# Performance work log

Hardware: AMD Instinct MI355X
Metric: run time of the kernel (lower is better)

Reference implementation:

```python
import jax, jax.numpy as jnp
import numpy as np

B, S, H = 2, 1024, 2048
NH, NKV, HD = 32, 8, 64
EPS = 1e-6
ROPE_BASE = 10000.0


def rms_norm(x, w, eps=EPS):
    xf = x.astype(jnp.float32)
    var = jnp.mean(xf * xf, axis=-1, keepdims=True)
    return (w * (xf * jax.lax.rsqrt(var + eps))).astype(x.dtype)


def rotate_half(x):
    x1, x2 = jnp.split(x, 2, axis=-1)
    return jnp.concatenate((-x2, x1), axis=-1)


def setup_inputs() -> dict:
    key = jax.random.key(0)
    ks = jax.random.split(key, 8)
    hidden_states = jax.random.normal(ks[0], (B, S, H), dtype=jnp.float32) * 0.02
    # real rotary embeddings for positions 0..S-1
    inv_freq = 1.0 / (ROPE_BASE ** (jnp.arange(0, HD, 2, dtype=jnp.float32) / HD))
    freqs = jnp.arange(S, dtype=jnp.float32)[:, None] * inv_freq[None, :]  # [S, HD/2]
    emb = jnp.concatenate((freqs, freqs), axis=-1)  # [S, HD]
    cos = jnp.broadcast_to(jnp.cos(emb)[None], (B, S, HD)).astype(jnp.float32)
    sin = jnp.broadcast_to(jnp.sin(emb)[None], (B, S, HD)).astype(jnp.float32)
    # additive causal mask [B, 1, S, S]
    causal = jnp.tril(jnp.ones((S, S), dtype=bool))
    attention_mask = jnp.broadcast_to(
        jnp.where(causal, 0.0, -1e9).astype(jnp.float32)[None, None], (B, 1, S, S))
    scale_in = 1.0 / np.sqrt(H)
    wq = jax.random.normal(ks[1], (H, NH * HD), dtype=jnp.float32) * scale_in
    wk = jax.random.normal(ks[2], (H, NKV * HD), dtype=jnp.float32) * scale_in
    wv = jax.random.normal(ks[3], (H, NKV * HD), dtype=jnp.float32) * scale_in
    wo = jax.random.normal(ks[4], (NH * HD, H), dtype=jnp.float32) * scale_in
    q_norm_w = jnp.ones((NH * HD,), dtype=jnp.float32)
    k_norm_w = jnp.ones((NKV * HD,), dtype=jnp.float32)
    return {"hidden_states": hidden_states, "cos": cos, "sin": sin,
            "attention_mask": attention_mask, "wq": wq, "wk": wk, "wv": wv,
            "wo": wo, "q_norm_w": q_norm_w, "k_norm_w": k_norm_w}


def reference(hidden_states, cos, sin, attention_mask, wq, wk, wv, wo, q_norm_w, k_norm_w):
    b, s, _ = hidden_states.shape
    scaling = HD ** -0.5
    groups = NH // NKV
    # projections + QK-norm (RMSNorm over full projected dim, before head split)
    q = rms_norm(hidden_states @ wq, q_norm_w)
    k = rms_norm(hidden_states @ wk, k_norm_w)
    v = hidden_states @ wv
    q = q.reshape(b, s, NH, HD).transpose(0, 2, 1, 3)   # [b, nh, s, hd]
    k = k.reshape(b, s, NKV, HD).transpose(0, 2, 1, 3)  # [b, nkv, s, hd]
    v = v.reshape(b, s, NKV, HD).transpose(0, 2, 1, 3)
    # RoPE (cos/sin broadcast over head dim)
    c = cos[:, None]  # [b, 1, s, hd]
    sn = sin[:, None]
    q = q * c + rotate_half(q) * sn
    k = k * c + rotate_half(k) * sn
    # GQA: repeat KV heads
    k = jnp.repeat(k, groups, axis=1)  # [b, nh, s, hd]
    v = jnp.repeat(v, groups, axis=1)
    scores = jnp.einsum('bhqd,bhkd->bhqk', q, k) * scaling + attention_mask
    attn = jax.nn.softmax(scores.astype(jnp.float32), axis=-1).astype(q.dtype)
    out = jnp.einsum('bhqk,bhkd->bhqd', attn, v)
    out = out.transpose(0, 2, 1, 3).reshape(b, s, NH * HD)
    return out @ wo
```

## Files before the change

kernel.cpp:

```cpp
#include <hip/hip_runtime.h>

#define B_    2
#define S_    1024
#define NH_   32
#define NKV_  8
#define T_    (B_*S_)

typedef unsigned short u16;
typedef unsigned int u32;
typedef __attribute__((ext_vector_type(8))) short bf16x8;
typedef __attribute__((ext_vector_type(4))) float f32x4;

__device__ __forceinline__ float bf2f(u16 u) {
    union { float f; unsigned int i; } c; c.i = ((unsigned int)u) << 16; return c.f;
}
__device__ __forceinline__ u16 f2bf(float f) {
    union { float f; unsigned int u; } c; c.f = f;
    return (u16)((c.u + 0x7FFFu + ((c.u >> 16) & 1u)) >> 16);
}

__device__ __forceinline__ void gld_lds16(const void* g, void* s) {
    __builtin_amdgcn_global_load_lds(
        (const __attribute__((address_space(1))) void*)g,
        (__attribute__((address_space(3))) void*)s,
        16, 0, 0);
}

__global__ __launch_bounds__(256) void preproc1(
    const float* __restrict__ hidden, const float* __restrict__ wq,
    const float* __restrict__ wk, const float* __restrict__ wv,
    const float* __restrict__ wo,
    u16* __restrict__ hidden_bf, u16* __restrict__ wqkvT, u16* __restrict__ woT)
{
    __shared__ float t[64][65];
    const int bid = blockIdx.x, tid = threadIdx.x;
    if (bid < 2048) {
        int i = (bid * 256 + tid) * 8;
        float4 v0 = *reinterpret_cast<const float4*>(&hidden[i]);
        float4 v1 = *reinterpret_cast<const float4*>(&hidden[i + 4]);
        u16 o[8] = { f2bf(v0.x), f2bf(v0.y), f2bf(v0.z), f2bf(v0.w),
                     f2bf(v1.x), f2bf(v1.y), f2bf(v1.z), f2bf(v1.w) };
        *reinterpret_cast<uint4*>(&hidden_bf[i]) = *reinterpret_cast<uint4*>(o);
        return;
    }
    const float* src; int scol, sN, n0, k0;
    u16* dst; int dK;
    if (bid < 3584) {
        const int tt = bid - 2048;
        n0 = (tt % 48) * 64; k0 = (tt / 48) * 64;
        if (n0 < 2048)      { src = wq; scol = n0;        sN = 2048; }
        else if (n0 < 2560) { src = wk; scol = n0 - 2048; sN = 512;  }
        else                { src = wv; scol = n0 - 2560; sN = 512;  }
        dst = wqkvT; dK = 2048;
    } else {
        const int tt = bid - 3584;
        n0 = (tt % 32) * 64; k0 = (tt / 32) * 64;
        src = wo; scol = n0; sN = 2048;
        dst = woT; dK = 2048;
    }
    #pragma unroll
    for (int i = 0; i < 16; ++i) {
        int e = i * 256 + tid, r = e >> 6, c = e & 63;
        t[r][c] = src[(size_t)(k0 + r) * sN + scol + c];
    }
    __syncthreads();
    #pragma unroll
    for (int i = 0; i < 16; ++i) {
        int e = i * 256 + tid, rr = e >> 6, cc = e & 63;
        dst[(size_t)(n0 + rr) * dK + k0 + cc] = f2bf(t[cc][rr]);
    }
}

template<bool OUT_BF16>
__global__ __launch_bounds__(256) void gemm_bt(
    const u16* __restrict__ A, const u16* __restrict__ Bt,
    void* __restrict__ Cv, int M, int N, int K)
{
    __shared__ u16 As[2][128 * 64];
    __shared__ u16 Bs[2][64 * 64];
    const int MB = M >> 7;
    const int cpx = gridDim.x >> 3;
    const int L = (blockIdx.x & 7) * cpx + (blockIdx.x >> 3);
    const int bm = (L % MB) * 128, bn = (L / MB) * 64;
    const int tid = threadIdx.x;
    const int w = tid >> 6, lane = tid & 63;
    const int wr = w >> 1, wc = w & 1;
    const int l15 = lane & 15, lg = lane >> 4;
    const int srow = lane >> 3;
    const int scolsw = (lane & 7) ^ srow;

    f32x4 acc[4][2] = {};
    const int nk = K >> 6;

#define GSTAGE(ks, bb) do {                                                    \
    const int kofs = (ks) * 64;                                                \
    _Pragma("unroll")                                                          \
    for (int i_ = 0; i_ < 4; ++i_) {                                           \
        int chunk_ = w * 4 + i_;                                               \
        int row_ = chunk_ * 8 + srow;                                          \
        gld_lds16(&A[(size_t)(bm + row_) * K + kofs + scolsw * 8],             \
                  &As[bb][chunk_ * 512]);                                      \
    }                                                                          \
    _Pragma("unroll")                                                          \
    for (int j_ = 0; j_ < 2; ++j_) {                                           \
        int chunk_ = w * 2 + j_;                                               \
        int row_ = chunk_ * 8 + srow;                                          \
        gld_lds16(&Bt[(size_t)(bn + row_) * K + kofs + scolsw * 8],            \
                  &Bs[bb][chunk_ * 512]);                                      \
    } } while (0)

    GSTAGE(0, 0);
    for (int ks = 0; ks < nk; ++ks) {
        const int cur = ks & 1;
        if (ks + 1 < nk) {
            GSTAGE(ks + 1, cur ^ 1);
            asm volatile("s_waitcnt vmcnt(6)" ::: "memory");
        } else {
            asm volatile("s_waitcnt vmcnt(0)" ::: "memory");
        }
        __builtin_amdgcn_sched_barrier(0);
        __builtin_amdgcn_s_barrier();
        __builtin_amdgcn_sched_barrier(0);

        #pragma unroll
        for (int kk = 0; kk < 2; ++kk) {
            const int phys = ((kk * 4 + lg) ^ (l15 & 7)) * 8;
            bf16x8 a[4], b[2];
            #pragma unroll
            for (int m = 0; m < 4; ++m)
                a[m] = *reinterpret_cast<const bf16x8*>(
                    &As[cur][(wr * 64 + m * 16 + l15) * 64 + phys]);
            #pragma unroll
            for (int n = 0; n < 2; ++n)
                b[n] = *reinterpret_cast<const bf16x8*>(
                    &Bs[cur][(wc * 32 + n * 16 + l15) * 64 + phys]);
            #pragma unroll
            for (int m = 0; m < 4; ++m)
                #pragma unroll
                for (int n = 0; n < 2; ++n)
                    acc[m][n] = __builtin_amdgcn_mfma_f32_16x16x32_bf16(
                        a[m], b[n], acc[m][n], 0, 0, 0);
        }
        __builtin_amdgcn_sched_barrier(0);
        __builtin_amdgcn_s_barrier();
    }
#undef GSTAGE

    const int orow0 = bm + wr * 64, ocol0 = bn + wc * 32;
    #pragma unroll
    for (int m = 0; m < 4; ++m)
        #pragma unroll
        for (int n = 0; n < 2; ++n)
            #pragma unroll
            for (int r = 0; r < 4; ++r) {
                int row = orow0 + m * 16 + lg * 4 + r;
                int col = ocol0 + n * 16 + l15;
                float v = acc[m][n][r];
                if (OUT_BF16)
                    ((u16*)Cv)[(size_t)row * N + col] = f2bf(v);
                else
                    ((float*)Cv)[(size_t)row * N + col] = v;
            }
}

template<int DIM>
__device__ __forceinline__ void rms_rope_row(
    u16* base, const float* __restrict__ w,
    const float* __restrict__ cs, const float* __restrict__ sn,
    float* row, float* red, int tid, float osc)
{
    float ss = 0.f;
    for (int i0 = tid * 8; i0 < DIM; i0 += 2048) {
        uint4 u = *reinterpret_cast<const uint4*>(&base[i0]);
        const u16* us = reinterpret_cast<const u16*>(&u);
        #pragma unroll
        for (int j = 0; j < 8; ++j) { float f = bf2f(us[j]); row[i0 + j] = f; ss += f * f; }
    }
    #pragma unroll
    for (int off = 1; off < 64; off <<= 1) ss += __shfl_xor(ss, off);
    if ((tid & 63) == 0) red[tid >> 6] = ss;
    __syncthreads();
    const float rstd = rsqrtf((red[0] + red[1] + red[2] + red[3]) * (1.0f / DIM) + 1e-6f);

    for (int i0 = tid * 8; i0 < DIM; i0 += 2048) {
        u16 o[8];
        #pragma unroll
        for (int j = 0; j < 8; ++j) {
            int i = i0 + j, dh = i & 63, bb = i & ~63;
            int oi = (dh < 32) ? bb + dh + 32 : bb + dh - 32;
            float y     = row[i]  * rstd * w[i];
            float other = row[oi] * rstd * w[oi];
            if (dh < 32) other = -other;
            o[j] = f2bf((y * cs[dh] + other * sn[dh]) * osc);
        }
        *reinterpret_cast<uint4*>(&base[i0]) = *reinterpret_cast<uint4*>(o);
    }
}

__global__ __launch_bounds__(256) void rmsnorm_rope_vt(
    u16* __restrict__ x, const float* __restrict__ qnw, const float* __restrict__ knw,
    const float* __restrict__ cosb, const float* __restrict__ sinb,
    u16* __restrict__ vT)
{
    __shared__ float smem[2304];
    const int bid = blockIdx.x, tid = threadIdx.x;
    if (bid < 2048) {
        const int t = bid;
        float* row = smem;
        float* red = smem + 2048;
        const float* cs = cosb + (size_t)t * 64;
        const float* sn = sinb + (size_t)t * 64;
        rms_rope_row<2048>(x + (size_t)t * 3072,        qnw, cs, sn, row, red, tid,
                           0.18033688f);
        __syncthreads();
        rms_rope_row<512 >(x + (size_t)t * 3072 + 2048, knw, cs, sn, row, red, tid,
                           1.0f);
        return;
    }
    u16 (*tu)[72] = reinterpret_cast<u16(*)[72]>(smem);
    const int bid2 = bid - 2048;
    const int hd = bid2 % 16;
    const int s0 = (bid2 / 16) * 64;
    const int b = hd >> 3, kvh = hd & 7;
    #pragma unroll
    for (int i = 0; i < 2; ++i) {
        int chunk = i * 256 + tid;
        int r = chunk >> 3, c8 = (chunk & 7) * 8;
        uint4 u = *reinterpret_cast<const uint4*>(
            &x[(size_t)(b * 1024 + s0 + r) * 3072 + 2560 + kvh * 64 + c8]);
        *reinterpret_cast<uint4*>(&tu[r][c8]) = u;
    }
    __syncthreads();
    #pragma unroll
    for (int i = 0; i < 2; ++i) {
        int chunk = i * 256 + tid;
        int d = chunk >> 3, c8 = (chunk & 7) * 8;
        u16 o[8];
        #pragma unroll
        for (int j = 0; j < 8; ++j) o[j] = tu[c8 + j][d];
        *reinterpret_cast<uint4*>(&vT[((size_t)(hd * 64 + d)) * 1024 + s0 + c8])
            = *reinterpret_cast<uint4*>(o);
    }
}

__global__ __launch_bounds__(256) void attn_tb(
    const u16* __restrict__ qkv,
    const u16* __restrict__ vT,
    u16* __restrict__ ob)
{
    __shared__ u16 Ks[3][64 * 64];
    __shared__ u16 Vs[3][64 * 64];
    __shared__ u16 Ps[4][16 * 64];

    const int bid = blockIdx.x;
    const int L   = (bid & 7) * 64 + (bid >> 3);
    const int g5  = L >> 5;
    const int rem = L & 31;
    const int ha  = rem & 3;
    const int p   = rem >> 2;
    const int b = g5 >> 3, kvh = g5 & 7;
    const int h = kvh * 4 + ha;
    const int qtA = p, qtB = 15 - p;

    const int tid = threadIdx.x, w = tid >> 6, lane = tid & 63;
    const int l15 = lane & 15, lg = lane >> 4;
    const int srow = lane >> 3;
    const int scolsw = (lane & 7) ^ srow;

    bf16x8 qfA[2], qfB[2];
    {
        const size_t rA = (size_t)(b * 1024 + qtA * 64 + w * 16 + l15);
        const size_t rB = (size_t)(b * 1024 + qtB * 64 + w * 16 + l15);
        #pragma unroll
        for (int kk = 0; kk < 2; ++kk) {
            qfA[kk] = *reinterpret_cast<const bf16x8*>(
                &qkv[rA * 3072 + h * 64 + kk * 32 + lg * 8]);
            qfB[kk] = *reinterpret_cast<const bf16x8*>(
                &qkv[rB * 3072 + h * 64 + kk * 32 + lg * 8]);
        }
    }
    asm volatile("s_waitcnt vmcnt(0)" ::: "memory");

    float lrA = 0.f, lrB = 0.f;
    f32x4 oaccA[4] = {}, oaccB[4] = {};

    const u16* kbase = qkv + 2048 + kvh * 64;
    const u16* vbase = vT + (size_t)(g5 * 64) * 1024;
    const int qgA = qtA * 64 + w * 16 + l15;
    const int qgB = qtB * 64 + w * 16 + l15;

#define ASTAGE(kt, bb) do {                                                    \
    _Pragma("unroll")                                                          \
    for (int i_ = 0; i_ < 2; ++i_) {                                           \
        int chunk_ = w * 2 + i_;                                               \
        int row_ = chunk_ * 8 + srow;                                          \
        gld_lds16(&kbase[(size_t)(b * 1024 + (kt) * 64 + row_) * 3072          \
                         + scolsw * 8], &Ks[bb][chunk_ * 512]);                \
        gld_lds16(&vbase[(size_t)row_ * 1024 + (kt) * 64 + scolsw * 8],        \
                  &Vs[bb][chunk_ * 512]);                                      \
    } } while (0)

    auto step = [&](int kt, int cur, const bf16x8 (&qf)[2],
                    float& lr, f32x4 (&oacc)[4], int qg, bool dz) {
        f32x4 sacc[4] = {};
        __builtin_amdgcn_s_setprio(1);
        #pragma unroll
        for (int kk = 0; kk < 2; ++kk) {
            const int phys = ((kk * 4 + lg) ^ (l15 & 7)) * 8;
            #pragma unroll
            for (int m = 0; m < 4; ++m) {
                bf16x8 kf = *reinterpret_cast<const bf16x8*>(
                    &Ks[cur][(m * 16 + l15) * 64 + phys]);
                sacc[m] = __builtin_amdgcn_mfma_f32_16x16x32_bf16(
                    kf, qf[kk], sacc[m], 0, 0, 0);
            }
        }
        __builtin_amdgcn_s_setprio(0);

        float ls = 0.f;
        #pragma unroll
        for (int m = 0; m < 4; ++m) {
            u16 pk[4];
            #pragma unroll
            for (int r = 0; r < 4; ++r) {
                float v = sacc[m][r];
                if (dz && (kt * 64 + m * 16 + lg * 4 + r > qg)) v = -1e30f;
                float e = exp2f(v);
                ls += e;
                pk[r] = f2bf(e);
            }
            const int keyc = m * 16 + lg * 4;
            const int phys = (keyc >> 3) ^ (l15 & 7);
            *reinterpret_cast<uint2*>(&Ps[w][l15 * 64 + phys * 8 + (keyc & 7)])
                = *reinterpret_cast<const uint2*>(pk);
        }
        lr += ls;

        __builtin_amdgcn_s_setprio(1);
        #pragma unroll
        for (int kk = 0; kk < 2; ++kk) {
            const int phys = ((kk * 4 + lg) ^ (l15 & 7)) * 8;
            bf16x8 pf = *reinterpret_cast<const bf16x8*>(
                &Ps[w][l15 * 64 + phys]);
            #pragma unroll
            for (int d = 0; d < 4; ++d) {
                bf16x8 vf = *reinterpret_cast<const bf16x8*>(
                    &Vs[cur][(d * 16 + l15) * 64 + phys]);
                oacc[d] = __builtin_amdgcn_mfma_f32_16x16x32_bf16(
                    pf, vf, oacc[d], 0, 0, 0);
            }
        }
        __builtin_amdgcn_s_setprio(0);
    };

    ASTAGE(0, 0);
    for (int s = 0; s <= 16; ++s) {
        const int cur = s % 3;
        if (s < 16) {
            const int ktn = (s + 1 <= p) ? (s + 1) : (s - p);
            ASTAGE(ktn, (s + 1) % 3);
            asm volatile("s_waitcnt vmcnt(4)" ::: "memory");
        } else {
            asm volatile("s_waitcnt vmcnt(0)" ::: "memory");
        }
        __builtin_amdgcn_sched_barrier(0);
        __builtin_amdgcn_s_barrier();
        __builtin_amdgcn_sched_barrier(0);

        if (s <= p) step(s,         cur, qfA, lrA, oaccA, qgA, s == p);
        else        step(s - p - 1, cur, qfB, lrB, oaccB, qgB, s == 16);
    }
#undef ASTAGE

    #pragma unroll
    for (int tt = 0; tt < 2; ++tt) {
        const int qt = tt ? qtB : qtA;
        float lsum = tt ? lrB : lrA;
        lsum += __shfl_xor(lsum, 16);
        lsum += __shfl_xor(lsum, 32);
        f32x4* oacc = tt ? oaccB : oaccA;
        float linv[4];
        #pragma unroll
        for (int r = 0; r < 4; ++r) {
            float lv = __shfl(lsum, (lane & 48) + ((lane >> 4) & 3) * 4 + r);
            linv[r] = 1.f / lv;
        }
        #pragma unroll
        for (int d = 0; d < 4; ++d)
            #pragma unroll
            for (int r = 0; r < 4; ++r)
                ob[(size_t)(b * 1024 + qt * 64 + w * 16 + lg * 4 + r) * 2048
                   + h * 64 + d * 16 + l15] = f2bf(oacc[d][r] * linv[r]);
    }
}

extern "C" void kernel_launch(void* const* d_in, const int* in_sizes, int n_in,
                              void* d_out, int out_size, void* d_ws, size_t ws_size,
                              hipStream_t stream)
{
    const float* hidden = (const float*)d_in[0];
    const float* cosb   = (const float*)d_in[1];
    const float* sinb   = (const float*)d_in[2];
    const float* wq     = (const float*)d_in[4];
    const float* wk     = (const float*)d_in[5];
    const float* wv     = (const float*)d_in[6];
    const float* wo     = (const float*)d_in[7];
    const float* qnw    = (const float*)d_in[8];
    const float* knw    = (const float*)d_in[9];
    float* out = (float*)d_out;

    char* ws = (char*)d_ws;
    u16* hidden_bf = (u16*)ws;
    u16* wqkvT     = (u16*)(ws + ((size_t)8  << 20));
    u16* attn_bf   = (u16*)(ws + ((size_t)8  << 20));
    u16* qkv_bf    = (u16*)(ws + ((size_t)20 << 20));
    u16* v_bfT     = (u16*)(ws + ((size_t)32 << 20));
    u16* woT       = (u16*)(ws + ((size_t)34 << 20));

    preproc1<<<4608, 256, 0, stream>>>(hidden, wq, wk, wv, wo,
                                       hidden_bf, wqkvT, woT);

    gemm_bt<true><<<768, 256, 0, stream>>>(hidden_bf, wqkvT, qkv_bf,
                                           2048, 3072, 2048);

    rmsnorm_rope_vt<<<2304, 256, 0, stream>>>(qkv_bf, qnw, knw, cosb, sinb, v_bfT);

    attn_tb<<<512, 256, 0, stream>>>(qkv_bf, v_bfT, attn_bf);

    gemm_bt<false><<<512, 256, 0, stream>>>(attn_bf, woT, out,
                                            2048, 2048, 2048);
}
```

Measured before the change: 125.2 us.

## Split attention KV loop into two halves with a separate merge kernel

The attention kernel's 17-step KV loop per block is split into two halves (steps 0-8 and 9-16), doubling the grid to 1024 blocks. Each half writes unnormalized fp32 partial outputs and row sums to workspace, and a new merge kernel adds them, normalizes, and converts to bf16. The K/V LDS ring shrinks from triple to double buffering, with an extra barrier per step. The aim is more parallelism and occupancy, at the cost of a large fp32 round trip through global memory and one more kernel launch.

```diff
diff --git a/kernel.cpp b/kernel.cpp
--- a/kernel.cpp
+++ b/kernel.cpp
@@ -243,24 +243,28 @@
     }
 }
 
-__global__ __launch_bounds__(256) void attn_tb(
+__global__ __launch_bounds__(256) void attn_split(
     const u16* __restrict__ qkv,
     const u16* __restrict__ vT,
-    u16* __restrict__ ob)
-{
-    __shared__ u16 Ks[3][64 * 64];
-    __shared__ u16 Vs[3][64 * 64];
+    float* __restrict__ opart,
+    float* __restrict__ lpart)
+{
+    __shared__ u16 Ks[2][64 * 64];
+    __shared__ u16 Vs[2][64 * 64];
     __shared__ u16 Ps[4][16 * 64];
 
     const int bid = blockIdx.x;
-    const int L   = (bid & 7) * 64 + (bid >> 3);
-    const int g5  = L >> 5;
-    const int rem = L & 31;
-    const int ha  = rem & 3;
-    const int p   = rem >> 2;
+    const int L    = (bid & 7) * 128 + (bid >> 3);
+    const int g5   = L >> 6;
+    const int rem  = L & 63;
+    const int ha   = rem & 3;
+    const int p    = (rem >> 2) & 7;
+    const int half = rem >> 5;
     const int b = g5 >> 3, kvh = g5 & 7;
     const int h = kvh * 4 + ha;
     const int qtA = p, qtB = 15 - p;
+    const int s0 = half ? 9 : 0;
+    const int s1 = half ? 17 : 9;
 
     const int tid = threadIdx.x, w = tid >> 6, lane = tid & 63;
     const int l15 = lane & 15, lg = lane >> 4;
@@ -353,12 +357,12 @@
         __builtin_amdgcn_s_setprio(0);
     };
 
-    ASTAGE(0, 0);
-    for (int s = 0; s <= 16; ++s) {
-        const int cur = s % 3;
-        if (s < 16) {
-            const int ktn = (s + 1 <= p) ? (s + 1) : (s - p);
-            ASTAGE(ktn, (s + 1) % 3);
+#define TILEOF(s) (((s) <= p) ? (s) : ((s) - p - 1))
+    ASTAGE(TILEOF(s0), s0 & 1);
+    for (int s = s0; s < s1; ++s) {
+        const int cur = s & 1;
+        if (s + 1 < s1) {
+            ASTAGE(TILEOF(s + 1), cur ^ 1);
             asm volatile("s_waitcnt vmcnt(4)" ::: "memory");
         } else {
             asm volatile("s_waitcnt vmcnt(0)" ::: "memory");
@@ -369,9 +373,15 @@
 
         if (s <= p) step(s,         cur, qfA, lrA, oaccA, qgA, s == p);
         else        step(s - p - 1, cur, qfB, lrB, oaccB, qgB, s == 16);
-    }
+
+        __builtin_amdgcn_sched_barrier(0);
+        __builtin_amdgcn_s_barrier();
+    }
+#undef TILEOF
 #undef ASTAGE
 
+    float* obase = opart + (size_t)half * (2048u * 2048u);
+    float* lbase = lpart + (size_t)half * (2048u * 32u);
     #pragma unroll
     for (int tt = 0; tt < 2; ++tt) {
         const int qt = tt ? qtB : qtA;
@@ -379,19 +389,39 @@
         lsum += __shfl_xor(lsum, 16);
         lsum += __shfl_xor(lsum, 32);
         f32x4* oacc = tt ? oaccB : oaccA;
-        float linv[4];
-        #pragma unroll
-        for (int r = 0; r < 4; ++r) {
-            float lv = __shfl(lsum, (lane & 48) + ((lane >> 4) & 3) * 4 + r);
-            linv[r] = 1.f / lv;
-        }
+        if ((lane >> 4) == 0)
+            lbase[(size_t)(b * 1024 + qt * 64 + w * 16 + l15) * 32 + h] = lsum;
         #pragma unroll
         for (int d = 0; d < 4; ++d)
             #pragma unroll
             for (int r = 0; r < 4; ++r)
-                ob[(size_t)(b * 1024 + qt * 64 + w * 16 + lg * 4 + r) * 2048
-                   + h * 64 + d * 16 + l15] = f2bf(oacc[d][r] * linv[r]);
-    }
+                obase[(size_t)(b * 1024 + qt * 64 + w * 16 + lg * 4 + r) * 2048
+                      + h * 64 + d * 16 + l15] = oacc[d][r];
+    }
+}
+
+__global__ __launch_bounds__(256) void attn_merge(
+    const float* __restrict__ opart, const float* __restrict__ lpart,
+    u16* __restrict__ ob)
+{
+    const int row = blockIdx.x, tid = threadIdx.x;
+    const int col = tid * 8;
+    const int h = col >> 6;
+    const float l0 = lpart[(size_t)row * 32 + h];
+    const float l1 = lpart[(size_t)(2048 + row) * 32 + h];
+    const float inv = 1.f / (l0 + l1);
+    const float* o0 = opart + (size_t)row * 2048 + col;
+    const float* o1 = o0 + (size_t)2048 * 2048;
+    float4 a0 = *reinterpret_cast<const float4*>(o0);
+    float4 a1 = *reinterpret_cast<const float4*>(o0 + 4);
+    float4 b0 = *reinterpret_cast<const float4*>(o1);
+    float4 b1 = *reinterpret_cast<const float4*>(o1 + 4);
+    u16 o[8] = { f2bf((a0.x + b0.x) * inv), f2bf((a0.y + b0.y) * inv),
+                 f2bf((a0.z + b0.z) * inv), f2bf((a0.w + b0.w) * inv),
+                 f2bf((a1.x + b1.x) * inv), f2bf((a1.y + b1.y) * inv),
+                 f2bf((a1.z + b1.z) * inv), f2bf((a1.w + b1.w) * inv) };
+    *reinterpret_cast<uint4*>(&ob[(size_t)row * 2048 + col])
+        = *reinterpret_cast<uint4*>(o);
 }
 
 extern "C" void kernel_launch(void* const* d_in, const int* in_sizes, int n_in,
@@ -416,6 +446,8 @@
     u16* qkv_bf    = (u16*)(ws + ((size_t)20 << 20));
     u16* v_bfT     = (u16*)(ws + ((size_t)32 << 20));
     u16* woT       = (u16*)(ws + ((size_t)34 << 20));
+    float* opart   = (float*)(ws + ((size_t)48 << 20));
+    float* lpart   = (float*)(ws + ((size_t)80 << 20));
 
     preproc1<<<4608, 256, 0, stream>>>(hidden, wq, wk, wv, wo,
                                        hidden_bf, wqkvT, woT);
@@ -425,7 +457,8 @@
 
     rmsnorm_rope_vt<<<2304, 256, 0, stream>>>(qkv_bf, qnw, knw, cosb, sinb, v_bfT);
 
-    attn_tb<<<512, 256, 0, stream>>>(qkv_bf, v_bfT, attn_bf);
+    attn_split<<<1024, 256, 0, stream>>>(qkv_bf, v_bfT, opart, lpart);
+    attn_merge<<<2048, 256, 0, stream>>>(opart, lpart, attn_bf);
 
     gemm_bt<false><<<512, 256, 0, stream>>>(attn_bf, woT, out,
                                             2048, 2048, 2048);
```

Result: slower. 132.2 us (+5.6%).
